# Kernel tuning notes

Measured on AMD Instinct MI355X. Metric: run time of the kernel, lower is better.

## Reference

```python
import jax, jax.numpy as jnp
import numpy as np

VOCAB, EMB, HID = 32000, 512, 1024


def setup_inputs() -> dict:
    key = jax.random.key(0)
    k1, k2, k3, k4, k5, k6 = jax.random.split(key, 6)
    sentences = jax.random.randint(k1, (64, 512), 0, VOCAB)
    emb_table = jax.random.normal(k2, (VOCAB, EMB), dtype=jnp.float32)
    s_ih = 1.0 / np.sqrt(HID)
    # PyTorch LSTM params: gate order (i, f, g, o)
    w_ih = jax.random.uniform(k3, (4 * HID, EMB), minval=-s_ih, maxval=s_ih, dtype=jnp.float32)
    w_hh = jax.random.uniform(k4, (4 * HID, HID), minval=-s_ih, maxval=s_ih, dtype=jnp.float32)
    b_ih = jax.random.uniform(k5, (4 * HID,), minval=-s_ih, maxval=s_ih, dtype=jnp.float32)
    b_hh = jax.random.uniform(k6, (4 * HID,), minval=-s_ih, maxval=s_ih, dtype=jnp.float32)
    return {"sentences": sentences, "emb_table": emb_table,
            "w_ih": w_ih, "w_hh": w_hh, "b_ih": b_ih, "b_hh": b_hh}


def _lstm_forward(emb_table, w_ih, w_hh, b_ih, b_hh, sentences):
    B = sentences.shape[0]
    H = w_hh.shape[1]
    # embedding lookup -> [T, B, E] (matches transpose(0,1) in torch code)
    embedded = emb_table[sentences].transpose(1, 0, 2)
    # precompute input projections for all timesteps: [T, B, 4H]
    x_gates = jnp.einsum('tbe,ge->tbg', embedded, w_ih) + b_ih + b_hh

    def step(carry, xg):
        h, c = carry
        gates = xg + h @ w_hh.T  # [B, 4H]
        i, f, g, o = jnp.split(gates, 4, axis=-1)
        i = jax.nn.sigmoid(i)
        f = jax.nn.sigmoid(f)
        g = jnp.tanh(g)
        o = jax.nn.sigmoid(o)
        c_new = f * c + i * g
        h_new = o * jnp.tanh(c_new)
        return (h_new, c_new), None

    h0 = jnp.zeros((B, H), dtype=emb_table.dtype)
    c0 = jnp.zeros((B, H), dtype=emb_table.dtype)
    (h, c), _ = jax.lax.scan(step, (h0, c0), x_gates)
    # original returns output of last step only: [1, B, H], and (h, c) each [1, B, H]
    return h[None], (h[None], c[None])


def reference(sentences, emb_table, w_ih, w_hh, b_ih, b_hh):
    output, (h, c) = _lstm_forward(emb_table, w_ih, w_hh, b_ih, b_hh, sentences)
    return output, h, c
```

## Files before the change

### kernel.cpp

```cpp
#include <hip/hip_runtime.h>

typedef __bf16 bf16x8 __attribute__((ext_vector_type(8)));
typedef float f32x4 __attribute__((ext_vector_type(4)));
typedef unsigned short u16;
typedef unsigned long long u64;

#define NSTEP 512

#define AL(p)   __hip_atomic_load((p), __ATOMIC_RELAXED, __HIP_MEMORY_SCOPE_AGENT)
#define AS(p,v) __hip_atomic_store((p), (v), __ATOMIC_RELAXED, __HIP_MEMORY_SCOPE_AGENT)

__device__ __forceinline__ u16 f2bf(float f) {
  union { float f; unsigned u; } x; x.f = f;
  return (u16)((x.u + 0x7fffu + ((x.u >> 16) & 1u)) >> 16);
}

__global__ void prep_kernel(u64* __restrict__ H0, int* __restrict__ F) {
  int i = blockIdx.x * blockDim.x + threadIdx.x;
  if (i < 16384) AS(H0 + i, 0ULL);
  if (i < 32768) AS(&F[i], 0);
}

__global__ void gather_kernel(const int* __restrict__ sent, const float* __restrict__ emb,
                              u16* __restrict__ A1) {
  int row = blockIdx.x * 4 + (threadIdx.x >> 6);
  int lane = threadIdx.x & 63;
  int t = row >> 6, b = row & 63;
  int idx = sent[b * 512 + t];
  const float* src = emb + (size_t)idx * 512 + lane * 8;
  u16* dst = A1 + (size_t)row * 512 + lane * 8;
  #pragma unroll
  for (int k = 0; k < 8; ++k) dst[k] = f2bf(src[k]);
}

__global__ void __launch_bounds__(256, 2)
lstm_kernel(const u16* __restrict__ A1,
            const float* __restrict__ wih, const float* __restrict__ whh,
            const float* __restrict__ bih, const float* __restrict__ bhh,
            u16* __restrict__ H, float* __restrict__ out, int* __restrict__ F) {
  __shared__ u16 wlds[48 * 16 * 36];
  __shared__ alignas(8) u16 hx[4][16][4];

  const int j   = blockIdx.x;
  const int tid = threadIdx.x;
  const int w   = tid >> 6;
  const int l   = tid & 63;
  const int lr  = l & 15, lk = l >> 4;
  const int g   = lr >> 2, nn = lr & 3;
  const int wrow = g * 1024 + j * 4 + nn;

  for (int task = tid; task < 3072; task += 256) {
    int kk = task >> 6;
    int rem = task & 63;
    int rb = rem >> 2, q = rem & 3;
    int row = (rb >> 2) * 1024 + j * 4 + (rb & 3);
    const float* src = (kk < 16) ? (wih + (size_t)row * 512 + kk * 32 + q * 8)
                                 : (whh + (size_t)row * 1024 + (kk - 16) * 32 + q * 8);
    u16* dst = wlds + (kk * 16 + rb) * 36 + q * 8;
    #pragma unroll
    for (int e = 0; e < 8; ++e) dst[e] = f2bf(src[e]);
  }
  __syncthreads();

  const float bias = bih[wrow] + bhh[wrow];
  const float sca = (g == 2) ? 2.f : 1.f;
  const float bd  = (g == 2) ? -1.f : 0.f;
  const int arow = w * 16 + lr;
  const u16* bx = wlds + lr * 36 + lk * 8;

  float cst[4] = {0.f, 0.f, 0.f, 0.f};

  bf16x8 ax[16];
  {
    const u16* apre = A1 + (size_t)arow * 512 + lk * 8;
    #pragma unroll
    for (int kk = 0; kk < 16; ++kk) ax[kk] = *(const bf16x8*)(apre + kk * 32);
  }

  union AF { bf16x8 v; u64 q[2]; };

#define WAITCH(c, T)                                                        \
  { const int* fp = F + ((c) * 64 + l) * 128 + w * 32;                      \
    while (AL(fp) < (T)) __builtin_amdgcn_s_sleep(1); }
#define LD8(BUF, CH)                                                        \
  { _Pragma("unroll")                                                       \
    for (int r = 0; r < 8; ++r)                                             \
      BUF[r].v = *(const bf16x8*)(hp + (CH) * 256 + r * 32); }
#define MM8(BUF, W0)                                                        \
  { _Pragma("unroll")                                                       \
    for (int r = 0; r < 8; ++r) {                                           \
      bf16x8 b = *(const bf16x8*)(bx + ((W0) + r) * 576);                   \
      acc = __builtin_amdgcn_mfma_f32_16x16x32_bf16(BUF[r].v, b, acc, 0, 0, 0); \
    } }

  #pragma unroll 1
  for (int t = 0; t < NSTEP; ++t) {
    AF ha[8], hb[8];
    const u16* hp = H + (size_t)t * 65536 + (size_t)arow * 1024 + lk * 8;
    WAITCH(0, t);
    LD8(ha, 0);
    WAITCH(1, t);
    LD8(hb, 1);
    f32x4 acc = { bias, bias, bias, bias };
    #pragma unroll
    for (int kk = 0; kk < 16; ++kk) {
      bf16x8 b = *(const bf16x8*)(bx + kk * 576);
      acc = __builtin_amdgcn_mfma_f32_16x16x32_bf16(ax[kk], b, acc, 0, 0, 0);
    }
    MM8(ha, 16);
    WAITCH(2, t); LD8(ha, 2);
    MM8(hb, 24);
    WAITCH(3, t); LD8(hb, 3);
    MM8(ha, 32);
    MM8(hb, 40);

    float hv4[4], cn4[4];
    #pragma unroll
    for (int r = 0; r < 4; ++r) {
      float xv = acc[r];
      float act = sca / (1.f + __expf(-sca * xv)) + bd;
      float gg = __shfl_xor(act, 8);
      float ff = __shfl_xor(act, 4);
      float oo = __shfl_xor(act, 12);
      float cn = ff * cst[r] + act * gg;
      cst[r] = cn;
      float tc = 2.f / (1.f + __expf(-2.f * cn)) - 1.f;
      hv4[r] = oo * tc;
      cn4[r] = cn;
    }

    if (t == NSTEP - 1) {
      if (lr < 4) {
        #pragma unroll
        for (int r = 0; r < 4; ++r) {
          int R = w * 16 + lk * 4 + r;
          out[(size_t)R * 1024 + j * 4 + lr]          = hv4[r];
          out[65536 + (size_t)R * 1024 + j * 4 + lr]  = hv4[r];
          out[131072 + (size_t)R * 1024 + j * 4 + lr] = cn4[r];
        }
      }
    } else {
      if (lr < 4) {
        #pragma unroll
        for (int r = 0; r < 4; ++r) hx[w][lk * 4 + r][lr] = f2bf(hv4[r]);
      }
      if (l < 16) {
        u64 pk = *(const u64*)(&hx[w][l][0]);
        u16* hw = H + (size_t)(t + 1) * 65536 + (size_t)(w * 16 + l) * 1024 + j * 4;
        AS((u64*)hw, pk);
      }
      asm volatile("s_waitcnt vmcnt(0)" ::: "memory");
      if (l == 0) AS(F + j * 128 + w * 32, t + 1);
      {
        const u16* apre = A1 + ((size_t)(t + 1) * 64 + arow) * 512 + lk * 8;
        #pragma unroll
        for (int kk = 0; kk < 16; ++kk) ax[kk] = *(const bf16x8*)(apre + kk * 32);
      }
    }
  }
#undef WAITCH
#undef LD8
#undef MM8
}

extern "C" void kernel_launch(void* const* d_in, const int* in_sizes, int n_in,
                              void* d_out, int out_size, void* d_ws, size_t ws_size,
                              hipStream_t stream) {
  const int*   sent = (const int*)d_in[0];
  const float* emb  = (const float*)d_in[1];
  const float* w_ih = (const float*)d_in[2];
  const float* w_hh = (const float*)d_in[3];
  const float* b_ih = (const float*)d_in[4];
  const float* b_hh = (const float*)d_in[5];
  float* out = (float*)d_out;

  char* ws = (char*)d_ws;
  u16* A1 = (u16*)ws;
  u16* H  = (u16*)(ws + 33554432);
  int* F  = (int*)(ws + 33554432 + 67108864);

  prep_kernel<<<256, 256, 0, stream>>>((u64*)H, F);
  gather_kernel<<<8192, 256, 0, stream>>>(sent, emb, A1);

  void* args[] = { (void*)&A1, (void*)&w_ih, (void*)&w_hh,
                   (void*)&b_ih, (void*)&b_hh, (void*)&H, (void*)&out, (void*)&F };
  hipError_t err = hipLaunchCooperativeKernel((void*)lstm_kernel, dim3(256), dim3(256),
                                              args, 0, stream);
  if (err != hipSuccess) {
    lstm_kernel<<<dim3(256), dim3(256), 0, stream>>>(A1, w_ih, w_hh, b_ih, b_hh,
                                                     H, out, F);
  }
}
```

Baseline: 4.319 ms.

## Repartition LSTM over 64 blocks with half of W_hh held in registers

Each workgroup now owns 16 hidden columns instead of 4, so the grid shrinks from 256 to 64 blocks of 512 threads. The input projection and first half of W_hh sit in dynamic LDS (about 144 KB), and the second half of W_hh stays in registers. The input-projection MFMAs are issued before the spin-wait on the flags, overlapping that work with the cross-block dependency. This cuts the number of flag producers per step and the chatter on the global barrier, at the cost of more per-block work on a critical path that is strictly serial, very high register pressure, and a large LDS footprint.

```diff
diff --git a/kernel.cpp b/kernel.cpp
--- a/kernel.cpp
+++ b/kernel.cpp
@@ -6,6 +6,7 @@
 typedef unsigned long long u64;
 
 #define NSTEP 512
+#define WLDS_BYTES 147456
 
 #define AL(p)   __hip_atomic_load((p), __ATOMIC_RELAXED, __HIP_MEMORY_SCOPE_AGENT)
 #define AS(p,v) __hip_atomic_store((p), (v), __ATOMIC_RELAXED, __HIP_MEMORY_SCOPE_AGENT)
@@ -18,7 +19,7 @@
 __global__ void prep_kernel(u64* __restrict__ H0, int* __restrict__ F) {
   int i = blockIdx.x * blockDim.x + threadIdx.x;
   if (i < 16384) AS(H0 + i, 0ULL);
-  if (i < 32768) AS(&F[i], 0);
+  if (i < 16384) AS(&F[i], 0);
 }
 
 __global__ void gather_kernel(const int* __restrict__ sent, const float* __restrict__ emb,
@@ -33,134 +34,158 @@
   for (int k = 0; k < 8; ++k) dst[k] = f2bf(src[k]);
 }
 
-__global__ void __launch_bounds__(256, 2)
+__global__ void __launch_bounds__(512, 1)
 lstm_kernel(const u16* __restrict__ A1,
             const float* __restrict__ wih, const float* __restrict__ whh,
             const float* __restrict__ bih, const float* __restrict__ bhh,
             u16* __restrict__ H, float* __restrict__ out, int* __restrict__ F) {
-  __shared__ u16 wlds[48 * 16 * 36];
-  __shared__ alignas(8) u16 hx[4][16][4];
+  extern __shared__ u16 wlds[];
+  __shared__ alignas(16) u16 hx[64][16];
 
   const int j   = blockIdx.x;
   const int tid = threadIdx.x;
-  const int w   = tid >> 6;
+  const int w8  = tid >> 6;
+  const int bt  = w8 >> 1;
+  const int cw  = w8 & 1;
   const int l   = tid & 63;
   const int lr  = l & 15, lk = l >> 4;
-  const int g   = lr >> 2, nn = lr & 3;
-  const int wrow = g * 1024 + j * 4 + nn;
-
-  for (int task = tid; task < 3072; task += 256) {
-    int kk = task >> 6;
-    int rem = task & 63;
+  const int g   = lr & 3, cc = lr >> 2;
+
+  for (int task = tid; task < 8192; task += 512) {
+    int kk = task >> 8;
+    int rem = task & 255;
     int rb = rem >> 2, q = rem & 3;
-    int row = (rb >> 2) * 1024 + j * 4 + (rb & 3);
+    int row = (rb & 3) * 1024 + j * 16 + (rb >> 2);
     const float* src = (kk < 16) ? (wih + (size_t)row * 512 + kk * 32 + q * 8)
                                  : (whh + (size_t)row * 1024 + (kk - 16) * 32 + q * 8);
-    u16* dst = wlds + (kk * 16 + rb) * 36 + q * 8;
+    u16* dst = wlds + (size_t)(kk * 64 + rb) * 36 + q * 8;
     #pragma unroll
     for (int e = 0; e < 8; ++e) dst[e] = f2bf(src[e]);
   }
+
+  const int col0 = cw * 8 + cc;
+  const int r0 = g * 1024 + j * 16 + col0;
+  const int r1 = r0 + 4;
+  bf16x8 wv0[16], wv1[16];
+  {
+    const float* p0 = whh + (size_t)r0 * 1024 + 512 + lk * 8;
+    const float* p1 = whh + (size_t)r1 * 1024 + 512 + lk * 8;
+    #pragma unroll
+    for (int c = 0; c < 16; ++c) {
+      union { bf16x8 v; u16 s[8]; } u0, u1;
+      #pragma unroll
+      for (int e = 0; e < 8; ++e) { u0.s[e] = f2bf(p0[c * 32 + e]); u1.s[e] = f2bf(p1[c * 32 + e]); }
+      wv0[c] = u0.v; wv1[c] = u1.v;
+    }
+  }
   __syncthreads();
 
-  const float bias = bih[wrow] + bhh[wrow];
+  const float bias0 = bih[r0] + bhh[r0];
+  const float bias1 = bih[r1] + bhh[r1];
   const float sca = (g == 2) ? 2.f : 1.f;
   const float bd  = (g == 2) ? -1.f : 0.f;
-  const int arow = w * 16 + lr;
-  const u16* bx = wlds + lr * 36 + lk * 8;
-
-  float cst[4] = {0.f, 0.f, 0.f, 0.f};
-
-  bf16x8 ax[16];
-  {
-    const u16* apre = A1 + (size_t)arow * 512 + lk * 8;
-    #pragma unroll
-    for (int kk = 0; kk < 16; ++kk) ax[kk] = *(const bf16x8*)(apre + kk * 32);
-  }
-
-  union AF { bf16x8 v; u64 q[2]; };
-
-#define WAITCH(c, T)                                                        \
-  { const int* fp = F + ((c) * 64 + l) * 128 + w * 32;                      \
-    while (AL(fp) < (T)) __builtin_amdgcn_s_sleep(1); }
-#define LD8(BUF, CH)                                                        \
-  { _Pragma("unroll")                                                       \
-    for (int r = 0; r < 8; ++r)                                             \
-      BUF[r].v = *(const bf16x8*)(hp + (CH) * 256 + r * 32); }
-#define MM8(BUF, W0)                                                        \
+  const int arow = bt * 16 + lr;
+  const u16* bxp = wlds + (size_t)(cw * 32 + lr) * 36 + lk * 8;
+
+  float cst0[4] = {0,0,0,0}, cst1[4] = {0,0,0,0};
+  bf16x8 ha[8], hb[8];
+
+#define LD8A(BUF, C0)                                                       \
+  { _Pragma("unroll")                                                       \
+    for (int r = 0; r < 8; ++r) BUF[r] = *(const bf16x8*)(ap + ((C0) + r) * 32); }
+#define LD8H(BUF, C0)                                                       \
+  { _Pragma("unroll")                                                       \
+    for (int r = 0; r < 8; ++r) BUF[r] = *(const bf16x8*)(hp + ((C0) + r) * 32); }
+#define MM8L(PA, PB, BUF, KK0)                                              \
   { _Pragma("unroll")                                                       \
     for (int r = 0; r < 8; ++r) {                                           \
-      bf16x8 b = *(const bf16x8*)(bx + ((W0) + r) * 576);                   \
-      acc = __builtin_amdgcn_mfma_f32_16x16x32_bf16(BUF[r].v, b, acc, 0, 0, 0); \
+      bf16x8 b0 = *(const bf16x8*)(bxp + (size_t)((KK0) + r) * 2304);       \
+      bf16x8 b1 = *(const bf16x8*)(bxp + (size_t)((KK0) + r) * 2304 + 576); \
+      PA = __builtin_amdgcn_mfma_f32_16x16x32_bf16(BUF[r], b0, PA, 0, 0, 0); \
+      PB = __builtin_amdgcn_mfma_f32_16x16x32_bf16(BUF[r], b1, PB, 0, 0, 0); \
+    } }
+#define MM8R(PA, PB, BUF, V0)                                               \
+  { _Pragma("unroll")                                                       \
+    for (int r = 0; r < 8; ++r) {                                           \
+      PA = __builtin_amdgcn_mfma_f32_16x16x32_bf16(BUF[r], wv0[(V0) + r], PA, 0, 0, 0); \
+      PB = __builtin_amdgcn_mfma_f32_16x16x32_bf16(BUF[r], wv1[(V0) + r], PB, 0, 0, 0); \
     } }
 
   #pragma unroll 1
   for (int t = 0; t < NSTEP; ++t) {
-    AF ha[8], hb[8];
+    int v0 = AL(F + (l * 8 + bt * 2 + 0) * 32);
+    int v1 = AL(F + (l * 8 + bt * 2 + 1) * 32);
+    const u16* ap = A1 + ((size_t)t * 64 + arow) * 512 + lk * 8;
+    f32x4 p0a = { bias0, bias0, bias0, bias0 };
+    f32x4 p1a = { bias1, bias1, bias1, bias1 };
+    f32x4 p0b = { 0.f, 0.f, 0.f, 0.f };
+    f32x4 p1b = { 0.f, 0.f, 0.f, 0.f };
+    LD8A(ha, 0); LD8A(hb, 8);
+    MM8L(p0a, p1a, ha, 0);
+    MM8L(p0b, p1b, hb, 8);
+    while (v0 < t) { __builtin_amdgcn_s_sleep(1); v0 = AL(F + (l * 8 + bt * 2 + 0) * 32); }
+    while (v1 < t) { __builtin_amdgcn_s_sleep(1); v1 = AL(F + (l * 8 + bt * 2 + 1) * 32); }
     const u16* hp = H + (size_t)t * 65536 + (size_t)arow * 1024 + lk * 8;
-    WAITCH(0, t);
-    LD8(ha, 0);
-    WAITCH(1, t);
-    LD8(hb, 1);
-    f32x4 acc = { bias, bias, bias, bias };
-    #pragma unroll
-    for (int kk = 0; kk < 16; ++kk) {
-      bf16x8 b = *(const bf16x8*)(bx + kk * 576);
-      acc = __builtin_amdgcn_mfma_f32_16x16x32_bf16(ax[kk], b, acc, 0, 0, 0);
-    }
-    MM8(ha, 16);
-    WAITCH(2, t); LD8(ha, 2);
-    MM8(hb, 24);
-    WAITCH(3, t); LD8(hb, 3);
-    MM8(ha, 32);
-    MM8(hb, 40);
-
-    float hv4[4], cn4[4];
+    LD8H(ha, 0); LD8H(hb, 8);
+    MM8L(p0a, p1a, ha, 16);
+    LD8H(ha, 16);
+    MM8L(p0b, p1b, hb, 24);
+    LD8H(hb, 24);
+    MM8R(p0a, p1a, ha, 0);
+    MM8R(p0b, p1b, hb, 8);
+
+    float hv0[4], cn0[4], hv1[4], cn1[4];
     #pragma unroll
     for (int r = 0; r < 4; ++r) {
-      float xv = acc[r];
-      float act = sca / (1.f + __expf(-sca * xv)) + bd;
-      float gg = __shfl_xor(act, 8);
-      float ff = __shfl_xor(act, 4);
-      float oo = __shfl_xor(act, 12);
-      float cn = ff * cst[r] + act * gg;
-      cst[r] = cn;
-      float tc = 2.f / (1.f + __expf(-2.f * cn)) - 1.f;
-      hv4[r] = oo * tc;
-      cn4[r] = cn;
+      float x0 = p0a[r] + p0b[r];
+      float x1 = p1a[r] + p1b[r];
+      float a0 = sca / (1.f + __expf(-sca * x0)) + bd;
+      float a1 = sca / (1.f + __expf(-sca * x1)) + bd;
+      float f0 = __shfl_xor(a0, 1), g0 = __shfl_xor(a0, 2), o0 = __shfl_xor(a0, 3);
+      float f1 = __shfl_xor(a1, 1), g1 = __shfl_xor(a1, 2), o1 = __shfl_xor(a1, 3);
+      float c0 = f0 * cst0[r] + a0 * g0;
+      float c1 = f1 * cst1[r] + a1 * g1;
+      cst0[r] = c0; cst1[r] = c1;
+      hv0[r] = o0 * (2.f / (1.f + __expf(-2.f * c0)) - 1.f);  cn0[r] = c0;
+      hv1[r] = o1 * (2.f / (1.f + __expf(-2.f * c1)) - 1.f);  cn1[r] = c1;
     }
 
     if (t == NSTEP - 1) {
-      if (lr < 4) {
+      if (g == 0) {
         #pragma unroll
         for (int r = 0; r < 4; ++r) {
-          int R = w * 16 + lk * 4 + r;
-          out[(size_t)R * 1024 + j * 4 + lr]          = hv4[r];
-          out[65536 + (size_t)R * 1024 + j * 4 + lr]  = hv4[r];
-          out[131072 + (size_t)R * 1024 + j * 4 + lr] = cn4[r];
+          int R = bt * 16 + lk * 4 + r;
+          int C = j * 16 + col0;
+          out[(size_t)R * 1024 + C]              = hv0[r];
+          out[65536 + (size_t)R * 1024 + C]      = hv0[r];
+          out[131072 + (size_t)R * 1024 + C]     = cn0[r];
+          out[(size_t)R * 1024 + C + 4]          = hv1[r];
+          out[65536 + (size_t)R * 1024 + C + 4]  = hv1[r];
+          out[131072 + (size_t)R * 1024 + C + 4] = cn1[r];
         }
       }
     } else {
-      if (lr < 4) {
+      if (g == 0) {
         #pragma unroll
-        for (int r = 0; r < 4; ++r) hx[w][lk * 4 + r][lr] = f2bf(hv4[r]);
+        for (int r = 0; r < 4; ++r) {
+          hx[bt * 16 + lk * 4 + r][cw * 8 + cc]     = f2bf(hv0[r]);
+          hx[bt * 16 + lk * 4 + r][cw * 8 + cc + 4] = f2bf(hv1[r]);
+        }
       }
       if (l < 16) {
-        u64 pk = *(const u64*)(&hx[w][l][0]);
-        u16* hw = H + (size_t)(t + 1) * 65536 + (size_t)(w * 16 + l) * 1024 + j * 4;
-        AS((u64*)hw, pk);
+        const u64* s = (const u64*)(&hx[bt * 16 + l][cw * 8]);
+        u64* hw = (u64*)(H + (size_t)(t + 1) * 65536
+                           + (size_t)(bt * 16 + l) * 1024 + j * 16 + cw * 8);
+        AS(hw, s[0]); AS(hw + 1, s[1]);
       }
       asm volatile("s_waitcnt vmcnt(0)" ::: "memory");
-      if (l == 0) AS(F + j * 128 + w * 32, t + 1);
-      {
-        const u16* apre = A1 + ((size_t)(t + 1) * 64 + arow) * 512 + lk * 8;
-        #pragma unroll
-        for (int kk = 0; kk < 16; ++kk) ax[kk] = *(const bf16x8*)(apre + kk * 32);
-      }
+      if (l == 0) AS(F + (j * 8 + w8) * 32, t + 1);
     }
   }
-#undef WAITCH
-#undef LD8
-#undef MM8
+#undef LD8A
+#undef LD8H
+#undef MM8L
+#undef MM8R
 }
 
 extern "C" void kernel_launch(void* const* d_in, const int* in_sizes, int n_in,
@@ -182,12 +207,15 @@
   prep_kernel<<<256, 256, 0, stream>>>((u64*)H, F);
   gather_kernel<<<8192, 256, 0, stream>>>(sent, emb, A1);
 
+  (void)hipFuncSetAttribute((const void*)lstm_kernel,
+                            hipFuncAttributeMaxDynamicSharedMemorySize, WLDS_BYTES);
+
   void* args[] = { (void*)&A1, (void*)&w_ih, (void*)&w_hh,
                    (void*)&b_ih, (void*)&b_hh, (void*)&H, (void*)&out, (void*)&F };
-  hipError_t err = hipLaunchCooperativeKernel((void*)lstm_kernel, dim3(256), dim3(256),
-                                              args, 0, stream);
+  hipError_t err = hipLaunchCooperativeKernel((void*)lstm_kernel, dim3(64), dim3(512),
+                                              args, WLDS_BYTES, stream);
   if (err != hipSuccess) {
-    lstm_kernel<<<dim3(256), dim3(256), 0, stream>>>(A1, w_ih, w_hh, b_ih, b_hh,
-                                                     H, out, F);
-  }
-}
+    lstm_kernel<<<dim3(64), dim3(512), WLDS_BYTES, stream>>>(A1, w_ih, w_hh,
+                                                             b_ih, b_hh, H, out, F);
+  }
+}
```

Measured after the change: 8.229 ms. 90.5% more time.
